# Kernel tuning notes

Measured on AMD Instinct MI355X. Metric: run time of the kernel, lower is better.

Reference implementation:

```python
import jax, jax.numpy as jnp
import numpy as np

EPS = 1e-5

def conv1x1(x, w, b):
    # x: [B,C,H,W], w: [O,C], b: [O]
    return jnp.einsum('bchw,oc->bohw', x, w) + b[None, :, None, None]

def bn(x, g, b, m, v):
    # eval-mode BatchNorm2d over channel axis 1
    s = g / jnp.sqrt(v + EPS)
    return (x - m[None, :, None, None]) * s[None, :, None, None] + b[None, :, None, None]

def setup_inputs() -> dict:
    key = jax.random.key(0)
    ks = jax.random.split(key, 12)
    B, C, Ci, H, W = 8, 512, 256, 64, 64
    d = {}
    d['x'] = jax.random.normal(ks[0], (B, C, H, W), jnp.float32)
    d['theta_w'] = jax.random.normal(ks[1], (Ci, C), jnp.float32) * (C ** -0.5)
    d['theta_b'] = jnp.zeros((Ci,), jnp.float32)
    d['theta_bn_g'] = jax.random.uniform(ks[2], (Ci,), jnp.float32, 0.5, 1.5)
    d['theta_bn_b'] = jax.random.normal(ks[3], (Ci,), jnp.float32) * 0.1
    d['theta_bn_m'] = jnp.zeros((Ci,), jnp.float32)
    d['theta_bn_v'] = jnp.ones((Ci,), jnp.float32)
    d['phi_w'] = jax.random.normal(ks[4], (Ci, C), jnp.float32) * (C ** -0.5)
    d['phi_b'] = jnp.zeros((Ci,), jnp.float32)
    d['phi_bn_g'] = jax.random.uniform(ks[5], (Ci,), jnp.float32, 0.5, 1.5)
    d['phi_bn_b'] = jax.random.normal(ks[6], (Ci,), jnp.float32) * 0.1
    d['phi_bn_m'] = jnp.zeros((Ci,), jnp.float32)
    d['phi_bn_v'] = jnp.ones((Ci,), jnp.float32)
    d['g_w'] = jax.random.normal(ks[7], (Ci, C), jnp.float32) * (C ** -0.5)
    d['g_b'] = jnp.zeros((Ci,), jnp.float32)
    d['wz_w'] = jax.random.normal(ks[8], (C, Ci), jnp.float32) * (Ci ** -0.5)
    d['wz_b'] = jnp.zeros((C,), jnp.float32)
    d['wz_bn_g'] = jax.random.uniform(ks[9], (C,), jnp.float32, 0.5, 1.5)
    d['wz_bn_b'] = jax.random.normal(ks[10], (C,), jnp.float32) * 0.1
    d['wz_bn_m'] = jnp.zeros((C,), jnp.float32)
    d['wz_bn_v'] = jnp.ones((C,), jnp.float32)
    return d

def reference(x, theta_w, theta_b, theta_bn_g, theta_bn_b, theta_bn_m, theta_bn_v,
              phi_w, phi_b, phi_bn_g, phi_bn_b, phi_bn_m, phi_bn_v,
              g_w, g_b, wz_w, wz_b, wz_bn_g, wz_bn_b, wz_bn_m, wz_bn_v):
    B, C, H, W = x.shape
    Ci = theta_w.shape[0]
    N = H * W
    scale = Ci ** -0.5
    th = bn(conv1x1(x, theta_w, theta_b), theta_bn_g, theta_bn_b, theta_bn_m, theta_bn_v).reshape(B, Ci, N)
    ph = bn(conv1x1(x, phi_w, phi_b), phi_bn_g, phi_bn_b, phi_bn_m, phi_bn_v).reshape(B, Ci, N)
    gx = conv1x1(x, g_w, g_b).reshape(B, Ci, N)
    # attn[b,n,m] = <theta[:,n], phi[:,m]> * scale, softmax over m (fp32 as in source)
    attn = jax.nn.softmax(jnp.einsum('bcn,bcm->bnm', th, ph) * scale, axis=-1)
    y = jnp.einsum('bnm,bcm->bcn', attn, gx).reshape(B, Ci, H, W)
    out = bn(conv1x1(y, wz_w, wz_b), wz_bn_g, wz_bn_b, wz_bn_m, wz_bn_v) + x
    return out
```

## Files before the change

kernel.cpp:

```cpp
#include <hip/hip_runtime.h>

typedef __attribute__((ext_vector_type(8))) short bf16x8;
typedef __attribute__((ext_vector_type(4))) float f32x4;
typedef __attribute__((ext_vector_type(16))) float f32x16;
typedef __attribute__((ext_vector_type(4))) unsigned short us4;
typedef __attribute__((ext_vector_type(8))) unsigned short us8;
typedef __attribute__((ext_vector_type(4))) unsigned int u32x4;

#define B_  8
#define C_  512
#define CI_ 256
#define N_  4096

__device__ __forceinline__ unsigned short f2b(float f) {
  unsigned u = __float_as_uint(f);
  u += 0x7FFFu + ((u >> 16) & 1u);
  return (unsigned short)(u >> 16);
}

__device__ __forceinline__ f32x4 mfma16(bf16x8 a, bf16x8 b, f32x4 c) {
  return __builtin_amdgcn_mfma_f32_16x16x32_bf16(a, b, c, 0, 0, 0);
}
__device__ __forceinline__ f32x16 mfma32(bf16x8 a, bf16x8 b, f32x16 c) {
  return __builtin_amdgcn_mfma_f32_32x32x16_bf16(a, b, c, 0, 0, 0);
}

__device__ __forceinline__ void gld16(const void* g, void* l) {
  __builtin_amdgcn_global_load_lds(
      (const __attribute__((address_space(1))) unsigned int*)g,
      (__attribute__((address_space(3))) unsigned int*)l, 16, 0, 0);
}

__device__ __forceinline__ unsigned cvt_pk_bf16(float lo, float hi) {
  unsigned r;
  asm("v_cvt_pk_bf16_f32 %0, %1, %2" : "=v"(r) : "v"(lo), "v"(hi));
  return r;
}

__global__ void fold_kernel(
  const float* __restrict__ thw, const float* __restrict__ thb,
  const float* __restrict__ thg, const float* __restrict__ thbb,
  const float* __restrict__ thm, const float* __restrict__ thv,
  const float* __restrict__ phw, const float* __restrict__ phb,
  const float* __restrict__ phg, const float* __restrict__ phbb,
  const float* __restrict__ phm, const float* __restrict__ phv,
  const float* __restrict__ gw,  const float* __restrict__ gb,
  const float* __restrict__ wzw, const float* __restrict__ wzb,
  const float* __restrict__ wzg, const float* __restrict__ wzbb,
  const float* __restrict__ wzm, const float* __restrict__ wzv,
  unsigned short* __restrict__ thW, unsigned short* __restrict__ phW,
  unsigned short* __restrict__ gW,  unsigned short* __restrict__ wzW,
  float* __restrict__ bTh, float* __restrict__ bPh,
  float* __restrict__ bG,  float* __restrict__ bWz)
{
  int i = blockIdx.x * 256 + threadIdx.x;
  const int WSZ = CI_ * C_;
  if (i < WSZ) { int o = i >> 9; thW[i] = f2b(thw[i] * (thg[o] * rsqrtf(thv[o] + 1e-5f))); return; }
  i -= WSZ;
  if (i < WSZ) { int o = i >> 9; phW[i] = f2b(phw[i] * (phg[o] * rsqrtf(phv[o] + 1e-5f))); return; }
  i -= WSZ;
  if (i < WSZ) { gW[i] = f2b(gw[i]); return; }
  i -= WSZ;
  if (i < WSZ) { int o = i >> 8; wzW[i] = f2b(wzw[i] * (wzg[o] * rsqrtf(wzv[o] + 1e-5f))); return; }
  i -= WSZ;
  if (i < CI_) { float s = thg[i] * rsqrtf(thv[i] + 1e-5f); bTh[i] = (thb[i] - thm[i]) * s + thbb[i]; return; }
  i -= CI_;
  if (i < CI_) { float s = phg[i] * rsqrtf(phv[i] + 1e-5f); bPh[i] = (phb[i] - phm[i]) * s + phbb[i]; return; }
  i -= CI_;
  if (i < CI_) { bG[i] = gb[i]; return; }
  i -= CI_;
  if (i < C_)  { float s = wzg[i] * rsqrtf(wzv[i] + 1e-5f); bWz[i] = (wzb[i] - wzm[i]) * s + wzbb[i]; return; }
}

__global__ __launch_bounds__(256) void transpose_cast(
  const float* __restrict__ x, unsigned short* __restrict__ xT)
{
  __shared__ float tl[64][68];
  const int b = blockIdx.z, c0 = blockIdx.y * 64, n0 = blockIdx.x * 64;
  const int t = threadIdx.x;
  const int r = t >> 2, q = (t & 3) * 16;
  const float* src = x + ((size_t)(b * C_ + c0 + r)) * N_ + n0 + q;
#pragma unroll
  for (int i = 0; i < 4; i++)
    *(f32x4*)&tl[r][q + i * 4] = *(const f32x4*)(src + i * 4);
  __syncthreads();
  unsigned short* dst = xT + ((size_t)(b * N_ + n0 + r)) * C_ + c0 + q;
  us8 o0, o1;
#pragma unroll
  for (int i = 0; i < 8; i++) o0[i] = f2b(tl[q + i][r]);
#pragma unroll
  for (int i = 0; i < 8; i++) o1[i] = f2b(tl[q + 8 + i][r]);
  *(us8*)dst = o0;
  *(us8*)(dst + 8) = o1;
}

template <int MODE>
__global__ __launch_bounds__(256, 2) void gemm_bt(
  const unsigned short* __restrict__ A,
  const unsigned short* __restrict__ Bm,
  const float* __restrict__ bias,
  const float* __restrict__ resid,
  void* __restrict__ outp,
  int Mdim, int Ndim, int Kdim)
{
  __shared__ __align__(16) unsigned short Al[2][128][64];
  __shared__ __align__(16) unsigned short Bl[2][128][64];
  const int b = blockIdx.z;
  const int m0 = blockIdx.y * 128;
  const int n0 = blockIdx.x * 128;
  const int t = threadIdx.x;
  const int w = t >> 6, l = t & 63, l15 = l & 15, g = l >> 4;
  const int wm = w >> 1, wn = w & 1;
  const int eg = l15 & 7;
  const unsigned short* Bb = Bm + (size_t)b * Ndim * Kdim;
  f32x4 acc[4][4];
#pragma unroll
  for (int i = 0; i < 4; i++)
#pragma unroll
    for (int j = 0; j < 4; j++) acc[i][j] = (f32x4){0.f, 0.f, 0.f, 0.f};

  int aoff[4], boff[4];
#pragma unroll
  for (int i = 0; i < 4; i++) {
    int j = w * 4 + i;
    int row = j * 8 + (l >> 3);
    int sw = ((l & 7) ^ (l >> 3)) * 8;
    aoff[i] = (m0 + row) * Kdim + sw;
    boff[i] = (n0 + row) * Kdim + sw;
  }

#define GSTAGE(bufv, k0v) do { \
    _Pragma("unroll") \
    for (int i_ = 0; i_ < 4; i_++) { \
      gld16(A  + aoff[i_] + (k0v), (unsigned char*)&Al[bufv][0][0] + (w * 4 + i_) * 1024); \
      gld16(Bb + boff[i_] + (k0v), (unsigned char*)&Bl[bufv][0][0] + (w * 4 + i_) * 1024); \
    } \
  } while (0)

  const int nk = Kdim >> 6;
  GSTAGE(0, 0);
  __syncthreads();
  for (int kk = 0; kk < nk; kk++) {
    if (kk + 1 < nk) GSTAGE((kk + 1) & 1, (kk + 1) * 64);
    const int cb = kk & 1;
#pragma unroll
    for (int ks = 0; ks < 2; ks++) {
      bf16x8 af[4], bfr[4];
#pragma unroll
      for (int i = 0; i < 4; i++)
        af[i]  = *(const bf16x8*)&Al[cb][wm * 64 + i * 16 + l15][((ks * 4 + g) ^ eg) * 8];
#pragma unroll
      for (int j = 0; j < 4; j++)
        bfr[j] = *(const bf16x8*)&Bl[cb][wn * 64 + j * 16 + l15][((ks * 4 + g) ^ eg) * 8];
#pragma unroll
      for (int i = 0; i < 4; i++)
#pragma unroll
        for (int j = 0; j < 4; j++)
          acc[i][j] = mfma16(af[i], bfr[j], acc[i][j]);
    }
    __syncthreads();
  }

#pragma unroll
  for (int i = 0; i < 4; i++) {
    int mrow = m0 + wm * 64 + i * 16 + 4 * g;
    f32x4 b4 = *(const f32x4*)&bias[mrow];
#pragma unroll
    for (int j = 0; j < 4; j++) {
      int n = n0 + wn * 64 + j * 16 + l15;
      f32x4 v = acc[i][j];
      v += b4;
      if constexpr (MODE == 0) {
        us4 pk = { f2b(v[0]), f2b(v[1]), f2b(v[2]), f2b(v[3]) };
        *(us4*)((unsigned short*)outp + ((size_t)b * Ndim + n) * Mdim + mrow) = pk;
      } else if constexpr (MODE == 1) {
        unsigned short* o = (unsigned short*)outp + ((size_t)b * Mdim + mrow) * (size_t)Ndim + n;
#pragma unroll
        for (int jj = 0; jj < 4; jj++) o[(size_t)jj * Ndim] = f2b(v[jj]);
      } else {
        size_t base = ((size_t)b * Mdim + mrow) * (size_t)Ndim + n;
        float* o = (float*)outp;
#pragma unroll
        for (int jj = 0; jj < 4; jj++)
          o[base + (size_t)jj * Ndim] = v[jj] + resid[base + (size_t)jj * Ndim];
      }
    }
  }
#undef GSTAGE
}

__global__ __launch_bounds__(512, 2) void attn_kernel(
  const unsigned short* __restrict__ thT,
  const unsigned short* __restrict__ phT,
  const unsigned short* __restrict__ gx,
  unsigned short* __restrict__ yT)
{
  __shared__ __align__(16) unsigned char lds[135168];
  const int t = threadIdx.x;
  const int w = t >> 6, l = t & 63, l31 = l & 31, h = l >> 5;
  const int qt = w & 3, mh = w >> 2;
  const int e7 = l31 & 7;
  const int id = blockIdx.x;
  const int b = id & 7;
  const int n0 = (id >> 3) * 128;
  const unsigned short* thB = thT + (size_t)b * N_ * CI_;
  const unsigned short* phB = phT + (size_t)b * N_ * CI_;
  const unsigned short* gxB = gx  + (size_t)b * CI_ * N_;

  const int kq = l >> 5, kc = l & 31;
  int koff[4];
#pragma unroll
  for (int i = 0; i < 4; i++) {
    int row = w * 8 + 2 * i + kq;
    koff[i] = row * 256 + ((kc ^ (row & 7)) * 8);
  }
  const int vq = l >> 3, vc = l & 7;
  int voff[4];
#pragma unroll
  for (int i = 0; i < 4; i++) {
    int ci = w * 32 + i * 8 + vq;
    voff[i] = ci * 4096 + ((vc ^ vq) * 8);
  }

#define STAGE(bufv, m0v) do { \
    const unsigned short* kg_ = phB + (size_t)(m0v) * 256; \
    const unsigned short* vg_ = gxB + (m0v); \
    unsigned base_ = (unsigned)(bufv) * 65536u + (unsigned)w * 4096u; \
    _Pragma("unroll") \
    for (int i_ = 0; i_ < 4; i_++) \
      gld16(kg_ + koff[i_], lds + base_ + i_ * 1024); \
    _Pragma("unroll") \
    for (int i_ = 0; i_ < 4; i_++) \
      gld16(vg_ + voff[i_], lds + base_ + 32768u + i_ * 1024); \
  } while (0)

  bf16x8 q[16];
  {
    const unsigned short* qp = thB + (size_t)(n0 + qt * 32 + l31) * CI_ + h * 8;
#pragma unroll
    for (int ks = 0; ks < 16; ks++) q[ks] = *(const bf16x8*)(qp + ks * 16);
  }

  f32x16 acc[8];
#pragma unroll
  for (int i = 0; i < 8; i++)
#pragma unroll
    for (int r = 0; r < 16; r++) acc[i][r] = 0.f;
  float M = -1e30f, L = 0.f;
  const float kS = 0.0625f * 1.44269504f;

  STAGE(0, 0);
  __syncthreads();
  int cur = 0;

  for (int tt = 0; tt < 64; tt++) {
    const int m0 = tt * 64;
    if (tt < 63) STAGE(cur ^ 1, m0 + 64);
    const unsigned char* kb = lds + cur * 65536;
    const unsigned char* vb = kb + 32768;

    f32x16 Sa, Sb;
#pragma unroll
    for (int r = 0; r < 16; r++) { Sa[r] = 0.f; Sb[r] = 0.f; }
#pragma unroll
    for (int ks = 0; ks < 16; ks += 2) {
      bf16x8 kf0 = *(const bf16x8*)(kb + (mh * 32 + l31) * 512 + ((((ks    ) * 2 + h)) ^ e7) * 16);
      bf16x8 kf1 = *(const bf16x8*)(kb + (mh * 32 + l31) * 512 + ((((ks + 1) * 2 + h)) ^ e7) * 16);
      Sa = mfma32(kf0, q[ks], Sa);
      Sb = mfma32(kf1, q[ks + 1], Sb);
    }
    f32x16 S = Sa + Sb;

    float m0t = fmaxf(fmaxf(S[0], S[1]),  fmaxf(S[2], S[3]));
    float m1t = fmaxf(fmaxf(S[4], S[5]),  fmaxf(S[6], S[7]));
    float m2t = fmaxf(fmaxf(S[8], S[9]),  fmaxf(S[10], S[11]));
    float m3t = fmaxf(fmaxf(S[12], S[13]), fmaxf(S[14], S[15]));
    float pm = fmaxf(fmaxf(m0t, m1t), fmaxf(m2t, m3t));
    pm *= kS;
    pm = fmaxf(pm, __shfl_xor(pm, 32));
    int dfr = __all(pm <= M + 8.0f);
    if (!dfr) {
      float nm = fmaxf(M, pm);
      float rs = exp2f(M - nm);
      M = nm; L *= rs;
#pragma unroll
      for (int r = 0; r < 16; r++) {
        float rr = __shfl(rs, h * 32 + ((r & 3) + 8 * (r >> 2) + 4 * h));
#pragma unroll
        for (int c = 0; c < 8; c++) acc[c][r] *= rr;
      }
    }
    float p[16];
#pragma unroll
    for (int r = 0; r < 16; r++) p[r] = exp2f(S[r] * kS - M);
    float s0t = (p[0] + p[1]) + (p[2] + p[3]);
    float s1t = (p[4] + p[5]) + (p[6] + p[7]);
    float s2t = (p[8] + p[9]) + (p[10] + p[11]);
    float s3t = (p[12] + p[13]) + (p[14] + p[15]);
    float rsum = (s0t + s1t) + (s2t + s3t);
    rsum += __shfl_xor(rsum, 32);
    L += rsum;

    unsigned pk[8];
#pragma unroll
    for (int qq = 0; qq < 8; qq++)
      pk[qq] = cvt_pk_bf16(p[2 * qq], p[2 * qq + 1]);

#pragma unroll
    for (int ks = 0; ks < 2; ks++) {
      unsigned s00 = pk[ks * 4 + 0], s10 = pk[ks * 4 + 2];
      unsigned s01 = pk[ks * 4 + 1], s11 = pk[ks * 4 + 3];
      unsigned own0 = h ? s10 : s00;
      unsigned snd0 = h ? s00 : s10;
      unsigned own1 = h ? s11 : s01;
      unsigned snd1 = h ? s01 : s11;
      unsigned sw0 = (unsigned)__shfl_xor((int)snd0, 32);
      unsigned sw1 = (unsigned)__shfl_xor((int)snd1, 32);
      u32x4 pv;
      pv[0] = h ? sw0 : own0;
      pv[1] = h ? sw1 : own1;
      pv[2] = h ? own0 : sw0;
      pv[3] = h ? own1 : sw1;
      bf16x8 pa = *(bf16x8*)&pv;
      const int gidx = mh * 4 + ks * 2 + h;
#pragma unroll
      for (int cit = 0; cit < 8; cit++) {
        bf16x8 vf = *(const bf16x8*)(vb + (cit * 32 + l31) * 128 + ((gidx ^ e7) << 4));
        acc[cit] = mfma32(pa, vf, acc[cit]);
      }
    }
    __syncthreads();
    cur ^= 1;
  }

  float* MB = (float*)(lds + 131072);
  float* LB = (float*)(lds + 131072 + 2048);
  MB[mh * 256 + qt * 64 + l] = M;
  LB[mh * 256 + qt * 64 + l] = L;
  float* ab = (float*)lds + qt * 8192 + l;
  if (mh) {
#pragma unroll
    for (int cit = 0; cit < 8; cit++)
#pragma unroll
      for (int r = 0; r < 16; r++)
        ab[(cit * 16 + r) * 64] = acc[cit][r];
  }
  __syncthreads();
  if (!mh) {
    unsigned short* yB = yT + (size_t)b * N_ * CI_;
#pragma unroll
    for (int r = 0; r < 16; r++) {
      int nl = (r & 3) + 8 * (r >> 2) + 4 * h;
      int li = qt * 64 + h * 32 + nl;
      float M1 = MB[li], L1 = LB[li];
      float M2 = MB[256 + li], L2 = LB[256 + li];
      float Mf = fmaxf(M1, M2);
      float s1 = exp2f(M1 - Mf), s2 = exp2f(M2 - Mf);
      float invf = 1.0f / (L1 * s1 + L2 * s2);
      s1 *= invf; s2 *= invf;
      int n = n0 + qt * 32 + nl;
#pragma unroll
      for (int cit = 0; cit < 8; cit++) {
        float v = acc[cit][r] * s1 + ab[(cit * 16 + r) * 64] * s2;
        yB[(size_t)n * CI_ + cit * 32 + l31] = f2b(v);
      }
    }
  }
#undef STAGE
}

extern "C" void kernel_launch(void* const* d_in, const int* in_sizes, int n_in,
                              void* d_out, int out_size, void* d_ws, size_t ws_size,
                              hipStream_t stream)
{
  const float* x    = (const float*)d_in[0];
  const float* thw  = (const float*)d_in[1];
  const float* thb  = (const float*)d_in[2];
  const float* thg  = (const float*)d_in[3];
  const float* thbb = (const float*)d_in[4];
  const float* thm  = (const float*)d_in[5];
  const float* thv  = (const float*)d_in[6];
  const float* phw  = (const float*)d_in[7];
  const float* phb  = (const float*)d_in[8];
  const float* phg  = (const float*)d_in[9];
  const float* phbb = (const float*)d_in[10];
  const float* phm  = (const float*)d_in[11];
  const float* phv  = (const float*)d_in[12];
  const float* gw   = (const float*)d_in[13];
  const float* gb   = (const float*)d_in[14];
  const float* wzw  = (const float*)d_in[15];
  const float* wzb  = (const float*)d_in[16];
  const float* wzg  = (const float*)d_in[17];
  const float* wzbb = (const float*)d_in[18];
  const float* wzm  = (const float*)d_in[19];
  const float* wzv  = (const float*)d_in[20];

  char* ws = (char*)d_ws;
  unsigned short* xbT = (unsigned short*)(ws);
  unsigned short* thT = (unsigned short*)(ws + 33554432ull);
  unsigned short* phT = (unsigned short*)(ws + 50331648ull);
  unsigned short* gxb = (unsigned short*)(ws + 67108864ull);
  unsigned short* yT  = (unsigned short*)(ws + 83886080ull);
  unsigned short* thW = (unsigned short*)(ws + 100663296ull);
  unsigned short* phW = (unsigned short*)(ws + 100925440ull);
  unsigned short* gW  = (unsigned short*)(ws + 101187584ull);
  unsigned short* wzW = (unsigned short*)(ws + 101449728ull);
  float* bTh = (float*)(ws + 101711872ull);
  float* bPh = (float*)(ws + 101712896ull);
  float* bG  = (float*)(ws + 101713920ull);
  float* bWz = (float*)(ws + 101714944ull);

  fold_kernel<<<2053, 256, 0, stream>>>(
      thw, thb, thg, thbb, thm, thv,
      phw, phb, phg, phbb, phm, phv,
      gw, gb, wzw, wzb, wzg, wzbb, wzm, wzv,
      thW, phW, gW, wzW, bTh, bPh, bG, bWz);

  transpose_cast<<<dim3(64, 8, 8), 256, 0, stream>>>(x, xbT);

  gemm_bt<0><<<dim3(32, 2, 8), 256, 0, stream>>>(thW, xbT, bTh, nullptr, thT, CI_, N_, C_);
  gemm_bt<0><<<dim3(32, 2, 8), 256, 0, stream>>>(phW, xbT, bPh, nullptr, phT, CI_, N_, C_);
  gemm_bt<1><<<dim3(32, 2, 8), 256, 0, stream>>>(gW,  xbT, bG,  nullptr, gxb, CI_, N_, C_);

  attn_kernel<<<dim3(256), 512, 0, stream>>>(thT, phT, gxb, yT);

  gemm_bt<2><<<dim3(32, 4, 8), 256, 0, stream>>>(wzW, yT, bWz, x, d_out, C_, N_, CI_);
}
```

Measured before the change: 327.8 us.

## Software-pipeline attention loop to overlap QK of next tile with PV

Restructures the flash-attention main loop so the QK^T MFMAs for tile t are interleaved with the P·V MFMAs for tile t-1, giving the matrix unit independent work while the softmax of the current tile is pending. K stays double-buffered, V becomes triple-buffered, and LDS grows to 160KB. Block-wide __syncthreads is replaced by raw s_barrier plus explicit vmcnt waits, so only a wave's own async LDS loads are waited on before reading data written by other waves, which risks races. The packed bf16 conversion intrinsic is also swapped for the software rounding helper, adding VALU work per tile.

```diff
diff --git a/kernel.cpp b/kernel.cpp
--- a/kernel.cpp
+++ b/kernel.cpp
@@ -29,12 +29,6 @@
   __builtin_amdgcn_global_load_lds(
       (const __attribute__((address_space(1))) unsigned int*)g,
       (__attribute__((address_space(3))) unsigned int*)l, 16, 0, 0);
-}
-
-__device__ __forceinline__ unsigned cvt_pk_bf16(float lo, float hi) {
-  unsigned r;
-  asm("v_cvt_pk_bf16_f32 %0, %1, %2" : "=v"(r) : "v"(lo), "v"(hi));
-  return r;
 }
 
 __global__ void fold_kernel(
@@ -195,7 +189,7 @@
   const unsigned short* __restrict__ gx,
   unsigned short* __restrict__ yT)
 {
-  __shared__ __align__(16) unsigned char lds[135168];
+  __shared__ __align__(16) unsigned char lds[163840];
   const int t = threadIdx.x;
   const int w = t >> 6, l = t & 63, l31 = l & 31, h = l >> 5;
   const int qt = w & 3, mh = w >> 2;
@@ -222,16 +216,17 @@
     voff[i] = ci * 4096 + ((vc ^ vq) * 8);
   }
 
-#define STAGE(bufv, m0v) do { \
+#define STAGE_K(slot, m0v) do { \
     const unsigned short* kg_ = phB + (size_t)(m0v) * 256; \
-    const unsigned short* vg_ = gxB + (m0v); \
-    unsigned base_ = (unsigned)(bufv) * 65536u + (unsigned)w * 4096u; \
     _Pragma("unroll") \
     for (int i_ = 0; i_ < 4; i_++) \
-      gld16(kg_ + koff[i_], lds + base_ + i_ * 1024); \
+      gld16(kg_ + koff[i_], lds + (unsigned)(slot) * 32768u + (unsigned)w * 4096u + i_ * 1024u); \
+  } while (0)
+#define STAGE_V(slot, m0v) do { \
+    const unsigned short* vg_ = gxB + (m0v); \
     _Pragma("unroll") \
     for (int i_ = 0; i_ < 4; i_++) \
-      gld16(vg_ + voff[i_], lds + base_ + 32768u + i_ * 1024); \
+      gld16(vg_ + voff[i_], lds + 65536u + (unsigned)(slot) * 32768u + (unsigned)w * 4096u + i_ * 1024u); \
   } while (0)
 
   bf16x8 q[16];
@@ -247,91 +242,114 @@
 #pragma unroll
     for (int r = 0; r < 16; r++) acc[i][r] = 0.f;
   float M = -1e30f, L = 0.f;
+  unsigned pkp[8];
   const float kS = 0.0625f * 1.44269504f;
 
-  STAGE(0, 0);
+#define SOFTMAX_UPDATE(Sv) do { \
+    float pm_ = Sv[0]; \
+    _Pragma("unroll") for (int r = 1; r < 16; r++) pm_ = fmaxf(pm_, Sv[r]); \
+    pm_ *= kS; \
+    pm_ = fmaxf(pm_, __shfl_xor(pm_, 32)); \
+    int dfr_ = __all(pm_ <= M + 8.0f); \
+    if (!dfr_) { \
+      float nm_ = fmaxf(M, pm_); \
+      float rs_ = exp2f(M - nm_); \
+      M = nm_; L *= rs_; \
+      _Pragma("unroll") for (int r = 0; r < 16; r++) { \
+        float rr_ = __shfl(rs_, h * 32 + ((r & 3) + 8 * (r >> 2) + 4 * h)); \
+        _Pragma("unroll") for (int c = 0; c < 8; c++) acc[c][r] *= rr_; \
+      } \
+    } \
+    float p_[16]; float rsum_ = 0.f; \
+    _Pragma("unroll") for (int r = 0; r < 16; r++) { p_[r] = exp2f(Sv[r] * kS - M); rsum_ += p_[r]; } \
+    rsum_ += __shfl_xor(rsum_, 32); \
+    L += rsum_; \
+    _Pragma("unroll") for (int qq = 0; qq < 8; qq++) \
+      pkp[qq] = ((unsigned)f2b(p_[2 * qq + 1]) << 16) | f2b(p_[2 * qq]); \
+  } while (0)
+
+#define BUILD_PA(pa0v, pa1v) do { \
+    u32x4 pv0_, pv1_; \
+    { unsigned s00 = pkp[0], s10 = pkp[2], s01 = pkp[1], s11 = pkp[3]; \
+      unsigned own0 = h ? s10 : s00, snd0 = h ? s00 : s10; \
+      unsigned own1 = h ? s11 : s01, snd1 = h ? s01 : s11; \
+      unsigned sw0 = (unsigned)__shfl_xor((int)snd0, 32); \
+      unsigned sw1 = (unsigned)__shfl_xor((int)snd1, 32); \
+      pv0_[0] = h ? sw0 : own0; pv0_[1] = h ? sw1 : own1; \
+      pv0_[2] = h ? own0 : sw0; pv0_[3] = h ? own1 : sw1; } \
+    { unsigned s00 = pkp[4], s10 = pkp[6], s01 = pkp[5], s11 = pkp[7]; \
+      unsigned own0 = h ? s10 : s00, snd0 = h ? s00 : s10; \
+      unsigned own1 = h ? s11 : s01, snd1 = h ? s01 : s11; \
+      unsigned sw0 = (unsigned)__shfl_xor((int)snd0, 32); \
+      unsigned sw1 = (unsigned)__shfl_xor((int)snd1, 32); \
+      pv1_[0] = h ? sw0 : own0; pv1_[1] = h ? sw1 : own1; \
+      pv1_[2] = h ? own0 : sw0; pv1_[3] = h ? own1 : sw1; } \
+    pa0v = *(bf16x8*)&pv0_; pa1v = *(bf16x8*)&pv1_; \
+  } while (0)
+
+  STAGE_K(0, 0); STAGE_V(0, 0);
+
+  __builtin_amdgcn_s_barrier();
+  STAGE_K(1, 64); STAGE_V(1, 64);
+  asm volatile("s_waitcnt vmcnt(8)" ::: "memory");
+  {
+    const unsigned char* kb = lds;
+    f32x16 S;
+#pragma unroll
+    for (int r = 0; r < 16; r++) S[r] = 0.f;
+#pragma unroll
+    for (int u = 0; u < 16; u++) {
+      bf16x8 kf = *(const bf16x8*)(kb + (mh * 32 + l31) * 512 + (((u * 2 + h)) ^ e7) * 16);
+      S = mfma32(kf, q[u], S);
+    }
+    SOFTMAX_UPDATE(S);
+  }
+
+  int vprev = 0, vstage = 2;
+  for (int tt = 1; tt < 64; tt++) {
+    __builtin_amdgcn_s_barrier();
+    if (tt < 63) {
+      STAGE_K((tt + 1) & 1, (tt + 1) * 64);
+      STAGE_V(vstage, (tt + 1) * 64);
+      asm volatile("s_waitcnt vmcnt(8)" ::: "memory");
+    } else {
+      asm volatile("s_waitcnt vmcnt(0)" ::: "memory");
+    }
+    const unsigned char* kb  = lds + (unsigned)(tt & 1) * 32768u;
+    const unsigned char* vbp = lds + 65536u + (unsigned)vprev * 32768u;
+
+    bf16x8 pa0, pa1;
+    BUILD_PA(pa0, pa1);
+
+    f32x16 S;
+#pragma unroll
+    for (int r = 0; r < 16; r++) S[r] = 0.f;
+#pragma unroll
+    for (int u = 0; u < 16; u++) {
+      bf16x8 kf = *(const bf16x8*)(kb + (mh * 32 + l31) * 512 + (((u * 2 + h)) ^ e7) * 16);
+      S = mfma32(kf, q[u], S);
+      const int ksv = u >> 3, cit = u & 7;
+      bf16x8 vf = *(const bf16x8*)(vbp + (cit * 32 + l31) * 128 + (((mh * 4 + ksv * 2 + h) ^ e7) << 4));
+      acc[cit] = mfma32(ksv ? pa1 : pa0, vf, acc[cit]);
+    }
+    SOFTMAX_UPDATE(S);
+    vprev  = (vprev  == 2) ? 0 : vprev + 1;
+    vstage = (vstage == 2) ? 0 : vstage + 1;
+  }
+
+  {
+    const unsigned char* vbp = lds + 65536u + (unsigned)vprev * 32768u;
+    bf16x8 pa0, pa1;
+    BUILD_PA(pa0, pa1);
+#pragma unroll
+    for (int ksv = 0; ksv < 2; ksv++)
+#pragma unroll
+      for (int cit = 0; cit < 8; cit++) {
+        bf16x8 vf = *(const bf16x8*)(vbp + (cit * 32 + l31) * 128 + (((mh * 4 + ksv * 2 + h) ^ e7) << 4));
+        acc[cit] = mfma32(ksv ? pa1 : pa0, vf, acc[cit]);
+      }
+  }
   __syncthreads();
-  int cur = 0;
-
-  for (int tt = 0; tt < 64; tt++) {
-    const int m0 = tt * 64;
-    if (tt < 63) STAGE(cur ^ 1, m0 + 64);
-    const unsigned char* kb = lds + cur * 65536;
-    const unsigned char* vb = kb + 32768;
-
-    f32x16 Sa, Sb;
-#pragma unroll
-    for (int r = 0; r < 16; r++) { Sa[r] = 0.f; Sb[r] = 0.f; }
-#pragma unroll
-    for (int ks = 0; ks < 16; ks += 2) {
-      bf16x8 kf0 = *(const bf16x8*)(kb + (mh * 32 + l31) * 512 + ((((ks    ) * 2 + h)) ^ e7) * 16);
-      bf16x8 kf1 = *(const bf16x8*)(kb + (mh * 32 + l31) * 512 + ((((ks + 1) * 2 + h)) ^ e7) * 16);
-      Sa = mfma32(kf0, q[ks], Sa);
-      Sb = mfma32(kf1, q[ks + 1], Sb);
-    }
-    f32x16 S = Sa + Sb;
-
-    float m0t = fmaxf(fmaxf(S[0], S[1]),  fmaxf(S[2], S[3]));
-    float m1t = fmaxf(fmaxf(S[4], S[5]),  fmaxf(S[6], S[7]));
-    float m2t = fmaxf(fmaxf(S[8], S[9]),  fmaxf(S[10], S[11]));
-    float m3t = fmaxf(fmaxf(S[12], S[13]), fmaxf(S[14], S[15]));
-    float pm = fmaxf(fmaxf(m0t, m1t), fmaxf(m2t, m3t));
-    pm *= kS;
-    pm = fmaxf(pm, __shfl_xor(pm, 32));
-    int dfr = __all(pm <= M + 8.0f);
-    if (!dfr) {
-      float nm = fmaxf(M, pm);
-      float rs = exp2f(M - nm);
-      M = nm; L *= rs;
-#pragma unroll
-      for (int r = 0; r < 16; r++) {
-        float rr = __shfl(rs, h * 32 + ((r & 3) + 8 * (r >> 2) + 4 * h));
-#pragma unroll
-        for (int c = 0; c < 8; c++) acc[c][r] *= rr;
-      }
-    }
-    float p[16];
-#pragma unroll
-    for (int r = 0; r < 16; r++) p[r] = exp2f(S[r] * kS - M);
-    float s0t = (p[0] + p[1]) + (p[2] + p[3]);
-    float s1t = (p[4] + p[5]) + (p[6] + p[7]);
-    float s2t = (p[8] + p[9]) + (p[10] + p[11]);
-    float s3t = (p[12] + p[13]) + (p[14] + p[15]);
-    float rsum = (s0t + s1t) + (s2t + s3t);
-    rsum += __shfl_xor(rsum, 32);
-    L += rsum;
-
-    unsigned pk[8];
-#pragma unroll
-    for (int qq = 0; qq < 8; qq++)
-      pk[qq] = cvt_pk_bf16(p[2 * qq], p[2 * qq + 1]);
-
-#pragma unroll
-    for (int ks = 0; ks < 2; ks++) {
-      unsigned s00 = pk[ks * 4 + 0], s10 = pk[ks * 4 + 2];
-      unsigned s01 = pk[ks * 4 + 1], s11 = pk[ks * 4 + 3];
-      unsigned own0 = h ? s10 : s00;
-      unsigned snd0 = h ? s00 : s10;
-      unsigned own1 = h ? s11 : s01;
-      unsigned snd1 = h ? s01 : s11;
-      unsigned sw0 = (unsigned)__shfl_xor((int)snd0, 32);
-      unsigned sw1 = (unsigned)__shfl_xor((int)snd1, 32);
-      u32x4 pv;
-      pv[0] = h ? sw0 : own0;
-      pv[1] = h ? sw1 : own1;
-      pv[2] = h ? own0 : sw0;
-      pv[3] = h ? own1 : sw1;
-      bf16x8 pa = *(bf16x8*)&pv;
-      const int gidx = mh * 4 + ks * 2 + h;
-#pragma unroll
-      for (int cit = 0; cit < 8; cit++) {
-        bf16x8 vf = *(const bf16x8*)(vb + (cit * 32 + l31) * 128 + ((gidx ^ e7) << 4));
-        acc[cit] = mfma32(pa, vf, acc[cit]);
-      }
-    }
-    __syncthreads();
-    cur ^= 1;
-  }
 
   float* MB = (float*)(lds + 131072);
   float* LB = (float*)(lds + 131072 + 2048);
@@ -366,7 +384,10 @@
       }
     }
   }
-#undef STAGE
+#undef STAGE_K
+#undef STAGE_V
+#undef SOFTMAX_UPDATE
+#undef BUILD_PA
 }
 
 extern "C" void kernel_launch(void* const* d_in, const int* in_sizes, int n_in,
```

Result: faster. 288.9 us (-11.9%).
